# Performance work log

Measured on AMD Instinct MI355X. Metric: run time of the kernel, lower is better.

The kernel has to match this reference:

```python
import jax, jax.numpy as jnp
import numpy as np

L, D_IN, D_HID, D_OUT, N = 8, 256, 1024, 256, 32768


def setup_inputs() -> dict:
    key = jax.random.key(0)
    kx, kp, kw1, kw2 = jax.random.split(key, 4)
    x = jax.random.normal(kx, (N, D_IN), dtype=jnp.float32)
    plane_idx = jax.random.randint(kp, (N,), 0, L, dtype=jnp.int32)
    W1 = jax.random.normal(kw1, (L, D_HID, D_IN), dtype=jnp.float32) * 0.014
    b1 = jnp.zeros((L, D_HID), dtype=jnp.float32)
    W2 = jax.random.normal(kw2, (L, D_OUT, D_HID), dtype=jnp.float32) * np.float32((2.0 / D_HID) ** 0.5)
    b2 = jnp.zeros((L, D_OUT), dtype=jnp.float32)
    return {"x": x, "W1": W1, "b1": b1, "W2": W2, "b2": b2, "plane_idx": plane_idx}


def reference(x, W1, b1, W2, b2, plane_idx):
    # Dense-dispatch MoE reference: scan over the L planes, run the full
    # 2-layer MLP for each plane's weights, and select per-walker rows via
    # the plane mask (equivalent math to gather -> MLP -> scatter).
    n_planes = W1.shape[0]
    out0 = jnp.zeros((x.shape[0], W2.shape[1]), dtype=x.dtype)

    def plane_step(out, p):
        h = jax.nn.gelu(x @ W1[p].T + b1[p], approximate=False)  # [N, D_hid]
        o = h @ W2[p].T + b2[p]                                  # [N, D_out]
        out = jnp.where((plane_idx == p)[:, None], o, out)
        return out, None

    out, _ = jax.lax.scan(plane_step, out0, jnp.arange(n_planes))
    return out
```

## Files before the change

### kernel.cpp

```cpp
#include <hip/hip_runtime.h>
#include <hip/hip_fp16.h>
#include <cstdint>

#define NT      32768
#define DIN     256
#define DHID    1024
#define DOUT    256
#define NPLANES 8
#define NBLK    (NT / 256)

typedef unsigned short u16;
typedef __attribute__((ext_vector_type(8))) _Float16 f16x8;
typedef __attribute__((ext_vector_type(4))) float    f32x4;

#define WS_OFFSETS 0
#define WS_META    64
#define WS_TP      1024
#define WS_TM      (WS_TP + 544*4)
#define WS_BLKHIST (WS_TM + 544*4)
#define WS_BLKBASE (WS_BLKHIST + NBLK*8*4)
#define WS_PERM    (WS_BLKBASE + NBLK*8*4)
#define WS_XB      (WS_PERM + NT*4)
#define WS_W1B     (WS_XB + NT*DIN*2)
#define WS_W2B     (WS_W1B + NPLANES*DHID*DIN*2)
#define WS_HB      (WS_W2B + NPLANES*DOUT*DHID*2)

__device__ __forceinline__ u16 f2h_bits(float f) {
    __half h = __float2half(f);
    return *reinterpret_cast<u16*>(&h);
}

__device__ __forceinline__ void gl_lds16(const void* g, void* l) {
    __builtin_amdgcn_global_load_lds(
        (const __attribute__((address_space(1))) void*)g,
        (__attribute__((address_space(3))) void*)l,
        16, 0, 0);
}

__device__ __forceinline__ float gelu_fast(float x) {
    const float u = x * (1.5957691216f + 0.07135481283f * x * x);
    const float e = __expf(-u);
    return x * __builtin_amdgcn_rcpf(1.0f + e);
}

__global__ void prep_k(const int* __restrict__ pidx, const float* __restrict__ x,
                       const float* __restrict__ W1, const float* __restrict__ W2,
                       int* __restrict__ blkhist, u16* __restrict__ xb,
                       u16* __restrict__ w1b, u16* __restrict__ w2b) {
    __shared__ int cnt[NPLANES];
    const int t = threadIdx.x, lane = t & 63;
    if ((int)blockIdx.x < NBLK) {
        if (t < NPLANES) cnt[t] = 0;
        __syncthreads();
        const int p = pidx[blockIdx.x * 256 + t];
#pragma unroll
        for (int q = 0; q < NPLANES; ++q) {
            unsigned long long m = __ballot(p == q);
            if (p == q && __popcll(m & ((1ULL << lane) - 1)) == 0)
                atomicAdd(&cnt[q], __popcll(m));
        }
        __syncthreads();
        if (t < NPLANES) blkhist[blockIdx.x * NPLANES + t] = cnt[t];
    }
    const int n0 = NT * DIN / 4, n1 = NPLANES * DHID * DIN / 4, n2 = NPLANES * DOUT * DHID / 4;
    const int stride = gridDim.x * blockDim.x;
    for (int i = blockIdx.x * blockDim.x + t; i < n0 + n1 + n2; i += stride) {
        const float4* s; ushort4* d; int j;
        if (i < n0)           { s = (const float4*)x;  d = (ushort4*)xb;  j = i; }
        else if (i < n0 + n1) { s = (const float4*)W1; d = (ushort4*)w1b; j = i - n0; }
        else                  { s = (const float4*)W2; d = (ushort4*)w2b; j = i - n0 - n1; }
        float4 v = s[j];
        ushort4 o;
        o.x = f2h_bits(v.x); o.y = f2h_bits(v.y);
        o.z = f2h_bits(v.z); o.w = f2h_bits(v.w);
        d[j] = o;
    }
}

__global__ void scan_k(const int* __restrict__ blkhist, int* __restrict__ offsets,
                       int* __restrict__ blkbase, int* __restrict__ meta,
                       int* __restrict__ tp, int* __restrict__ tm) {
    __shared__ int tot[NPLANES];
    const int t = threadIdx.x;
    if (t < NPLANES) {
        int s = 0;
#pragma unroll 8
        for (int b = 0; b < NBLK; ++b) s += blkhist[b * NPLANES + t];
        tot[t] = s;
    }
    __syncthreads();
    if (t == 0) {
        int off = 0, tc = 0;
        for (int p = 0; p < NPLANES; ++p) {
            offsets[p] = off;
            for (int m = 0; m < tot[p]; m += 64) { tp[tc] = p; tm[tc] = m; ++tc; }
            off += tot[p];
        }
        offsets[NPLANES] = off;
        meta[0] = tc;
    }
    __syncthreads();
    if (t < NPLANES) {
        int run = offsets[t];
#pragma unroll 8
        for (int b = 0; b < NBLK; ++b) {
            blkbase[b * NPLANES + t] = run;
            run += blkhist[b * NPLANES + t];
        }
    }
}

__global__ void scatter_k(const int* __restrict__ pidx, const int* __restrict__ blkbase,
                          int* __restrict__ perm) {
    __shared__ int wcnt[4][NPLANES];
    __shared__ int wbase[4][NPLANES];
    const int t = threadIdx.x, lane = t & 63, wave = t >> 6;
    const int i = blockIdx.x * 256 + t;
    const int p = pidx[i];
    int rank = 0;
#pragma unroll
    for (int q = 0; q < NPLANES; ++q) {
        unsigned long long m = __ballot(p == q);
        if (lane == 0) wcnt[wave][q] = __popcll(m);
        if (p == q) rank = __popcll(m & ((1ULL << lane) - 1));
    }
    __syncthreads();
    if (t < NPLANES) {
        int run = blkbase[blockIdx.x * NPLANES + t];
#pragma unroll
        for (int w = 0; w < 4; ++w) { wbase[w][t] = run; run += wcnt[w][t]; }
    }
    __syncthreads();
    perm[wbase[wave][p] + rank] = i;
}

#define XCD_MAP(NSPLIT, NW)                                                    \
    const int ntiles = meta[0];                                                \
    const int xcd = blockIdx.x & 7, idx = blockIdx.x >> 3;                     \
    const int q8 = ntiles >> 3, r8 = ntiles & 7;                               \
    const int tn = q8 + (xcd < r8 ? 1 : 0);                                    \
    if (idx >= tn * (NSPLIT)) return;                                          \
    const int tile = (xcd < r8 ? xcd * (q8 + 1)                                \
                               : r8 * (q8 + 1) + (xcd - r8) * q8)              \
                     + idx / (NSPLIT);                                         \
    const int n0v = (idx % (NSPLIT)) * (NW);

__global__ __launch_bounds__(256, 4) void gemm1_k(
    const u16* __restrict__ xb, const u16* __restrict__ w1b,
    const float* __restrict__ b1, const int* __restrict__ perm,
    const int* __restrict__ offsets, const int* __restrict__ meta,
    const int* __restrict__ tp, const int* __restrict__ tm,
    u16* __restrict__ hb)
{
    __shared__ __align__(16) u16 smem[20480];
    XCD_MAP(4, 256)
    const int p   = tp[tile];
    const int m0  = tm[tile];
    const int off = offsets[p];
    const int cnt = offsets[p + 1] - off;

    u16* const sA = smem;
    u16* const sB = smem + 4096;

    const int tid = threadIdx.x, srow = tid >> 3, sch = tid & 7;
    const u16* aptr[2];
#pragma unroll
    for (int c = 0; c < 2; ++c) {
        const int row = c * 32 + srow;
        const int gr  = min(m0 + row, cnt - 1);
        aptr[c] = xb + (size_t)perm[off + gr] * DIN + ((sch ^ (srow & 7)) * 8);
    }
    const u16* bptr[8];
#pragma unroll
    for (int c = 0; c < 8; ++c) {
        const int row = c * 32 + srow;
        bptr[c] = w1b + ((size_t)p * DHID + n0v + row) * DIN + ((sch ^ (srow & 7)) * 8);
    }
    const int wave = tid >> 6, lane = tid & 63;
    const int wc = wave;
    const int lm = lane & 15, lk = lane >> 4;

    f32x4 acc[4][4];
#pragma unroll
    for (int a = 0; a < 4; ++a)
#pragma unroll
        for (int b = 0; b < 4; ++b) acc[a][b] = (f32x4){0.f, 0.f, 0.f, 0.f};

    for (int kt = 0; kt < DIN / 64; ++kt) {
        const int k0 = kt * 64;
#pragma unroll
        for (int c = 0; c < 2; ++c) gl_lds16(aptr[c] + k0, sA + c * 2048 + tid * 8);
#pragma unroll
        for (int c = 0; c < 8; ++c) gl_lds16(bptr[c] + k0, sB + c * 2048 + tid * 8);
        __syncthreads();
#pragma unroll
        for (int kk = 0; kk < 2; ++kk) {
            const int g = kk * 4 + lk;
            f16x8 af[4];
#pragma unroll
            for (int mf = 0; mf < 4; ++mf) {
                const int row = mf * 16 + lm;
                af[mf] = *(const f16x8*)(sA + row * 64 + ((g ^ (row & 7)) * 8));
            }
#pragma unroll
            for (int nf = 0; nf < 4; ++nf) {
                const int row = wc * 64 + nf * 16 + lm;
                const f16x8 bf = *(const f16x8*)(sB + row * 64 + ((g ^ (row & 7)) * 8));
#pragma unroll
                for (int mf = 0; mf < 4; ++mf)
                    acc[mf][nf] = __builtin_amdgcn_mfma_f32_16x16x32_f16(
                        af[mf], bf, acc[mf][nf], 0, 0, 0);
            }
        }
        __syncthreads();
    }

    u16* const sOut = smem;
#pragma unroll
    for (int nf = 0; nf < 4; ++nf) {
        const int col = wc * 64 + nf * 16 + lm;
        const float bb = b1[p * DHID + n0v + col];
        const int cc = col >> 3, c7 = col & 7;
#pragma unroll
        for (int mf = 0; mf < 4; ++mf) {
#pragma unroll
            for (int j = 0; j < 4; ++j) {
                const int tok = mf * 16 + lk * 4 + j;
                sOut[tok * 256 + ((cc ^ (tok & 31)) * 8) + c7] =
                    f2h_bits(gelu_fast(acc[mf][nf][j] + bb));
            }
        }
    }
    __syncthreads();
    const int r = tid >> 2, qq = tid & 3;
    if (m0 + r < cnt) {
        u16* dst = hb + (size_t)(off + m0 + r) * DHID + n0v;
#pragma unroll
        for (int c = 0; c < 8; ++c) {
            const int l = qq * 8 + c;
            *(int4*)(dst + l * 8) = *(const int4*)(sOut + r * 256 + ((l ^ (r & 31)) * 8));
        }
    }
}

__global__ __launch_bounds__(256, 4) void gemm2_k(
    const u16* __restrict__ hb, const u16* __restrict__ w2b,
    const float* __restrict__ b2, const int* __restrict__ perm,
    const int* __restrict__ offsets, const int* __restrict__ meta,
    const int* __restrict__ tp, const int* __restrict__ tm,
    float* __restrict__ out)
{
    __shared__ __align__(16) u16 smem[12288];
    XCD_MAP(2, 128)
    const int p   = tp[tile];
    const int m0  = tm[tile];
    const int off = offsets[p];
    const int cnt = offsets[p + 1] - off;

    u16* const sA = smem;
    u16* const sB = smem + 4096;

    const int tid = threadIdx.x;
    const u16* aptr[2];
    const u16* bptr[4];
#pragma unroll
    for (int c = 0; c < 2; ++c) {
        const int slot = c * 256 + tid, row = slot >> 3, ch = slot & 7;
        aptr[c] = hb + (size_t)(off + min(m0 + row, cnt - 1)) * DHID + ((ch ^ (row & 7)) * 8);
    }
#pragma unroll
    for (int c = 0; c < 4; ++c) {
        const int slot = c * 256 + tid, row = slot >> 3, ch = slot & 7;
        bptr[c] = w2b + ((size_t)p * DOUT + n0v + row) * DHID + ((ch ^ (row & 7)) * 8);
    }
    const int wave = tid >> 6, lane = tid & 63;
    const int wr = wave >> 1, wc = wave & 1;
    const int lm = lane & 15, lk = lane >> 4;

    f32x4 acc[2][4];
#pragma unroll
    for (int a = 0; a < 2; ++a)
#pragma unroll
        for (int b = 0; b < 4; ++b) acc[a][b] = (f32x4){0.f, 0.f, 0.f, 0.f};

    for (int kt = 0; kt < DHID / 64; ++kt) {
        const int k0 = kt * 64;
#pragma unroll
        for (int c = 0; c < 2; ++c) gl_lds16(aptr[c] + k0, sA + c * 2048 + tid * 8);
#pragma unroll
        for (int c = 0; c < 4; ++c) gl_lds16(bptr[c] + k0, sB + c * 2048 + tid * 8);
        __syncthreads();
#pragma unroll
        for (int kk = 0; kk < 2; ++kk) {
            f16x8 af[2], bf[4];
#pragma unroll
            for (int mf = 0; mf < 2; ++mf) {
                const int row = wr * 32 + mf * 16 + lm;
                const int g   = kk * 4 + lk;
                af[mf] = *(const f16x8*)(sA + row * 64 + ((g ^ (row & 7)) * 8));
            }
#pragma unroll
            for (int nf = 0; nf < 4; ++nf) {
                const int row = wc * 64 + nf * 16 + lm;
                const int g   = kk * 4 + lk;
                bf[nf] = *(const f16x8*)(sB + row * 64 + ((g ^ (row & 7)) * 8));
            }
#pragma unroll
            for (int mf = 0; mf < 2; ++mf)
#pragma unroll
                for (int nf = 0; nf < 4; ++nf)
                    acc[mf][nf] = __builtin_amdgcn_mfma_f32_16x16x32_f16(
                        af[mf], bf[nf], acc[mf][nf], 0, 0, 0);
        }
        __syncthreads();
    }

#pragma unroll
    for (int nf = 0; nf < 4; ++nf) {
        const int col = n0v + wc * 64 + nf * 16 + lm;
        const float bb = b2[p * DOUT + col];
#pragma unroll
        for (int mf = 0; mf < 2; ++mf) {
#pragma unroll
            for (int j = 0; j < 4; ++j) {
                const int tok = wr * 32 + mf * 16 + lk * 4 + j;
                if (m0 + tok < cnt)
                    out[(size_t)perm[off + m0 + tok] * DOUT + col] = acc[mf][nf][j] + bb;
            }
        }
    }
}

extern "C" void kernel_launch(void* const* d_in, const int* in_sizes, int n_in,
                              void* d_out, int out_size, void* d_ws, size_t ws_size,
                              hipStream_t stream) {
    const float* x    = (const float*)d_in[0];
    const float* W1   = (const float*)d_in[1];
    const float* b1   = (const float*)d_in[2];
    const float* W2   = (const float*)d_in[3];
    const float* b2   = (const float*)d_in[4];
    const int*   pidx = (const int*)d_in[5];
    float*       out  = (float*)d_out;

    char* ws      = (char*)d_ws;
    int* offsets  = (int*)(ws + WS_OFFSETS);
    int* meta     = (int*)(ws + WS_META);
    int* tp       = (int*)(ws + WS_TP);
    int* tm       = (int*)(ws + WS_TM);
    int* blkhist  = (int*)(ws + WS_BLKHIST);
    int* blkbase  = (int*)(ws + WS_BLKBASE);
    int* perm     = (int*)(ws + WS_PERM);
    u16* xb       = (u16*)(ws + WS_XB);
    u16* w1b      = (u16*)(ws + WS_W1B);
    u16* w2b      = (u16*)(ws + WS_W2B);
    u16* hb       = (u16*)(ws + WS_HB);

    prep_k<<<2048, 256, 0, stream>>>(pidx, x, W1, W2, blkhist, xb, w1b, w2b);
    scan_k<<<1, 64, 0, stream>>>(blkhist, offsets, blkbase, meta, tp, tm);
    scatter_k<<<NBLK, 256, 0, stream>>>(pidx, blkbase, perm);

    gemm1_k<<<2080, 256, 0, stream>>>(xb, w1b, b1, perm, offsets, meta, tp, tm, hb);
    gemm2_k<<<1040, 256, 0, stream>>>(hb, w2b, b2, perm, offsets, meta, tp, tm, out);
}
```

Baseline: 117.7 us.

## Split-K GEMM2 with atomic accumulation and narrower GEMM1 tiles

```diff
diff --git a/kernel.cpp b/kernel.cpp
--- a/kernel.cpp
+++ b/kernel.cpp
@@ -134,7 +134,7 @@
     perm[wbase[wave][p] + rank] = i;
 }
 
-#define XCD_MAP(NSPLIT, NW)                                                    \
+#define XCD_MAP_HDR(NSPLIT)                                                    \
     const int ntiles = meta[0];                                                \
     const int xcd = blockIdx.x & 7, idx = blockIdx.x >> 3;                     \
     const int q8 = ntiles >> 3, r8 = ntiles & 7;                               \
@@ -143,17 +143,18 @@
     const int tile = (xcd < r8 ? xcd * (q8 + 1)                                \
                                : r8 * (q8 + 1) + (xcd - r8) * q8)              \
                      + idx / (NSPLIT);                                         \
-    const int n0v = (idx % (NSPLIT)) * (NW);
-
-__global__ __launch_bounds__(256, 4) void gemm1_k(
+    const int sub = idx % (NSPLIT);
+
+__global__ __launch_bounds__(256, 6) void gemm1_k(
     const u16* __restrict__ xb, const u16* __restrict__ w1b,
     const float* __restrict__ b1, const int* __restrict__ perm,
     const int* __restrict__ offsets, const int* __restrict__ meta,
     const int* __restrict__ tp, const int* __restrict__ tm,
     u16* __restrict__ hb)
 {
-    __shared__ __align__(16) u16 smem[20480];
-    XCD_MAP(4, 256)
+    __shared__ __align__(16) u16 smem[12288];
+    XCD_MAP_HDR(8)
+    const int n0v = sub * 128;
     const int p   = tp[tile];
     const int m0  = tm[tile];
     const int off = offsets[p];
@@ -162,27 +163,27 @@
     u16* const sA = smem;
     u16* const sB = smem + 4096;
 
-    const int tid = threadIdx.x, srow = tid >> 3, sch = tid & 7;
+    const int tid = threadIdx.x;
     const u16* aptr[2];
+    const u16* bptr[4];
 #pragma unroll
     for (int c = 0; c < 2; ++c) {
-        const int row = c * 32 + srow;
-        const int gr  = min(m0 + row, cnt - 1);
-        aptr[c] = xb + (size_t)perm[off + gr] * DIN + ((sch ^ (srow & 7)) * 8);
-    }
-    const u16* bptr[8];
-#pragma unroll
-    for (int c = 0; c < 8; ++c) {
-        const int row = c * 32 + srow;
-        bptr[c] = w1b + ((size_t)p * DHID + n0v + row) * DIN + ((sch ^ (srow & 7)) * 8);
+        const int slot = c * 256 + tid, row = slot >> 3, ch = slot & 7;
+        const int gr = min(m0 + row, cnt - 1);
+        aptr[c] = xb + (size_t)perm[off + gr] * DIN + ((ch ^ (row & 7)) * 8);
+    }
+#pragma unroll
+    for (int c = 0; c < 4; ++c) {
+        const int slot = c * 256 + tid, row = slot >> 3, ch = slot & 7;
+        bptr[c] = w1b + ((size_t)p * DHID + n0v + row) * DIN + ((ch ^ (row & 7)) * 8);
     }
     const int wave = tid >> 6, lane = tid & 63;
-    const int wc = wave;
+    const int wr = wave >> 1, wc = wave & 1;
     const int lm = lane & 15, lk = lane >> 4;
 
-    f32x4 acc[4][4];
-#pragma unroll
-    for (int a = 0; a < 4; ++a)
+    f32x4 acc[2][4];
+#pragma unroll
+    for (int a = 0; a < 2; ++a)
 #pragma unroll
         for (int b = 0; b < 4; ++b) acc[a][b] = (f32x4){0.f, 0.f, 0.f, 0.f};
 
@@ -191,26 +192,29 @@
 #pragma unroll
         for (int c = 0; c < 2; ++c) gl_lds16(aptr[c] + k0, sA + c * 2048 + tid * 8);
 #pragma unroll
-        for (int c = 0; c < 8; ++c) gl_lds16(bptr[c] + k0, sB + c * 2048 + tid * 8);
+        for (int c = 0; c < 4; ++c) gl_lds16(bptr[c] + k0, sB + c * 2048 + tid * 8);
         __syncthreads();
 #pragma unroll
         for (int kk = 0; kk < 2; ++kk) {
-            const int g = kk * 4 + lk;
-            f16x8 af[4];
-#pragma unroll
-            for (int mf = 0; mf < 4; ++mf) {
-                const int row = mf * 16 + lm;
+            f16x8 af[2], bf[4];
+#pragma unroll
+            for (int mf = 0; mf < 2; ++mf) {
+                const int row = wr * 32 + mf * 16 + lm;
+                const int g   = kk * 4 + lk;
                 af[mf] = *(const f16x8*)(sA + row * 64 + ((g ^ (row & 7)) * 8));
             }
 #pragma unroll
             for (int nf = 0; nf < 4; ++nf) {
                 const int row = wc * 64 + nf * 16 + lm;
-                const f16x8 bf = *(const f16x8*)(sB + row * 64 + ((g ^ (row & 7)) * 8));
-#pragma unroll
-                for (int mf = 0; mf < 4; ++mf)
+                const int g   = kk * 4 + lk;
+                bf[nf] = *(const f16x8*)(sB + row * 64 + ((g ^ (row & 7)) * 8));
+            }
+#pragma unroll
+            for (int mf = 0; mf < 2; ++mf)
+#pragma unroll
+                for (int nf = 0; nf < 4; ++nf)
                     acc[mf][nf] = __builtin_amdgcn_mfma_f32_16x16x32_f16(
-                        af[mf], bf, acc[mf][nf], 0, 0, 0);
-            }
+                        af[mf], bf[nf], acc[mf][nf], 0, 0, 0);
         }
         __syncthreads();
     }
@@ -222,11 +226,11 @@
         const float bb = b1[p * DHID + n0v + col];
         const int cc = col >> 3, c7 = col & 7;
 #pragma unroll
-        for (int mf = 0; mf < 4; ++mf) {
+        for (int mf = 0; mf < 2; ++mf) {
 #pragma unroll
             for (int j = 0; j < 4; ++j) {
-                const int tok = mf * 16 + lk * 4 + j;
-                sOut[tok * 256 + ((cc ^ (tok & 31)) * 8) + c7] =
+                const int tok = wr * 32 + mf * 16 + lk * 4 + j;
+                sOut[tok * 128 + ((cc ^ (tok & 15)) * 8) + c7] =
                     f2h_bits(gelu_fast(acc[mf][nf][j] + bb));
             }
         }
@@ -236,9 +240,9 @@
     if (m0 + r < cnt) {
         u16* dst = hb + (size_t)(off + m0 + r) * DHID + n0v;
 #pragma unroll
-        for (int c = 0; c < 8; ++c) {
-            const int l = qq * 8 + c;
-            *(int4*)(dst + l * 8) = *(const int4*)(sOut + r * 256 + ((l ^ (r & 31)) * 8));
+        for (int c = 0; c < 4; ++c) {
+            const int l = qq * 4 + c;
+            *(int4*)(dst + l * 8) = *(const int4*)(sOut + r * 128 + ((l ^ (r & 15)) * 8));
         }
     }
 }
@@ -250,82 +254,83 @@
     const int* __restrict__ tp, const int* __restrict__ tm,
     float* __restrict__ out)
 {
-    __shared__ __align__(16) u16 smem[12288];
-    XCD_MAP(2, 128)
+    __shared__ __align__(16) u16 smem[20480];
+    XCD_MAP_HDR(4)
+    const int seg = sub;
     const int p   = tp[tile];
     const int m0  = tm[tile];
     const int off = offsets[p];
     const int cnt = offsets[p + 1] - off;
+    const int kbase = seg * 256;
 
     u16* const sA = smem;
     u16* const sB = smem + 4096;
 
-    const int tid = threadIdx.x;
+    const int tid = threadIdx.x, srow = tid >> 3, sch = tid & 7;
     const u16* aptr[2];
-    const u16* bptr[4];
 #pragma unroll
     for (int c = 0; c < 2; ++c) {
-        const int slot = c * 256 + tid, row = slot >> 3, ch = slot & 7;
-        aptr[c] = hb + (size_t)(off + min(m0 + row, cnt - 1)) * DHID + ((ch ^ (row & 7)) * 8);
-    }
-#pragma unroll
-    for (int c = 0; c < 4; ++c) {
-        const int slot = c * 256 + tid, row = slot >> 3, ch = slot & 7;
-        bptr[c] = w2b + ((size_t)p * DOUT + n0v + row) * DHID + ((ch ^ (row & 7)) * 8);
+        const int row = c * 32 + srow;
+        const int gr  = min(m0 + row, cnt - 1);
+        aptr[c] = hb + (size_t)(off + gr) * DHID + kbase + ((sch ^ (srow & 7)) * 8);
+    }
+    const u16* bptr[8];
+#pragma unroll
+    for (int c = 0; c < 8; ++c) {
+        const int row = c * 32 + srow;
+        bptr[c] = w2b + ((size_t)p * DOUT + row) * DHID + kbase + ((sch ^ (srow & 7)) * 8);
     }
     const int wave = tid >> 6, lane = tid & 63;
-    const int wr = wave >> 1, wc = wave & 1;
+    const int wc = wave;
     const int lm = lane & 15, lk = lane >> 4;
 
-    f32x4 acc[2][4];
-#pragma unroll
-    for (int a = 0; a < 2; ++a)
+    f32x4 acc[4][4];
+#pragma unroll
+    for (int a = 0; a < 4; ++a)
 #pragma unroll
         for (int b = 0; b < 4; ++b) acc[a][b] = (f32x4){0.f, 0.f, 0.f, 0.f};
 
-    for (int kt = 0; kt < DHID / 64; ++kt) {
+    for (int kt = 0; kt < 4; ++kt) {
         const int k0 = kt * 64;
 #pragma unroll
         for (int c = 0; c < 2; ++c) gl_lds16(aptr[c] + k0, sA + c * 2048 + tid * 8);
 #pragma unroll
-        for (int c = 0; c < 4; ++c) gl_lds16(bptr[c] + k0, sB + c * 2048 + tid * 8);
+        for (int c = 0; c < 8; ++c) gl_lds16(bptr[c] + k0, sB + c * 2048 + tid * 8);
         __syncthreads();
 #pragma unroll
         for (int kk = 0; kk < 2; ++kk) {
-            f16x8 af[2], bf[4];
-#pragma unroll
-            for (int mf = 0; mf < 2; ++mf) {
-                const int row = wr * 32 + mf * 16 + lm;
-                const int g   = kk * 4 + lk;
+            const int g = kk * 4 + lk;
+            f16x8 af[4];
+#pragma unroll
+            for (int mf = 0; mf < 4; ++mf) {
+                const int row = mf * 16 + lm;
                 af[mf] = *(const f16x8*)(sA + row * 64 + ((g ^ (row & 7)) * 8));
             }
 #pragma unroll
             for (int nf = 0; nf < 4; ++nf) {
                 const int row = wc * 64 + nf * 16 + lm;
-                const int g   = kk * 4 + lk;
-                bf[nf] = *(const f16x8*)(sB + row * 64 + ((g ^ (row & 7)) * 8));
-            }
-#pragma unroll
-            for (int mf = 0; mf < 2; ++mf)
-#pragma unroll
-                for (int nf = 0; nf < 4; ++nf)
+                const f16x8 bf = *(const f16x8*)(sB + row * 64 + ((g ^ (row & 7)) * 8));
+#pragma unroll
+                for (int mf = 0; mf < 4; ++mf)
                     acc[mf][nf] = __builtin_amdgcn_mfma_f32_16x16x32_f16(
-                        af[mf], bf[nf], acc[mf][nf], 0, 0, 0);
+                        af[mf], bf, acc[mf][nf], 0, 0, 0);
+            }
         }
         __syncthreads();
     }
 
 #pragma unroll
     for (int nf = 0; nf < 4; ++nf) {
-        const int col = n0v + wc * 64 + nf * 16 + lm;
-        const float bb = b2[p * DOUT + col];
-#pragma unroll
-        for (int mf = 0; mf < 2; ++mf) {
+        const int col = wc * 64 + nf * 16 + lm;
+        const float bb = (seg == 0) ? b2[p * DOUT + col] : 0.0f;
+#pragma unroll
+        for (int mf = 0; mf < 4; ++mf) {
 #pragma unroll
             for (int j = 0; j < 4; ++j) {
-                const int tok = wr * 32 + mf * 16 + lk * 4 + j;
+                const int tok = mf * 16 + lk * 4 + j;
                 if (m0 + tok < cnt)
-                    out[(size_t)perm[off + m0 + tok] * DOUT + col] = acc[mf][nf][j] + bb;
+                    atomicAdd(&out[(size_t)perm[off + m0 + tok] * DOUT + col],
+                              acc[mf][nf][j] + bb);
             }
         }
     }
@@ -355,10 +360,12 @@
     u16* w2b      = (u16*)(ws + WS_W2B);
     u16* hb       = (u16*)(ws + WS_HB);
 
+    hipMemsetAsync(out, 0, (size_t)out_size * sizeof(float), stream);
+
     prep_k<<<2048, 256, 0, stream>>>(pidx, x, W1, W2, blkhist, xb, w1b, w2b);
     scan_k<<<1, 64, 0, stream>>>(blkhist, offsets, blkbase, meta, tp, tm);
     scatter_k<<<NBLK, 256, 0, stream>>>(pidx, blkbase, perm);
 
-    gemm1_k<<<2080, 256, 0, stream>>>(xb, w1b, b1, perm, offsets, meta, tp, tm, hb);
-    gemm2_k<<<1040, 256, 0, stream>>>(hb, w2b, b2, perm, offsets, meta, tp, tm, out);
-}
+    gemm1_k<<<4352, 256, 0, stream>>>(xb, w1b, b1, perm, offsets, meta, tp, tm, hb);
+    gemm2_k<<<2176, 256, 0, stream>>>(hb, w2b, b2, perm, offsets, meta, tp, tm, out);
+}
```

Measured after the change: 215.8 us. +83.4%, slower.
